# Kernel optimization log

Hardware: AMD Instinct MI355X
Metric: run time of the kernel (lower is better)

## Reference

```python
import jax, jax.numpy as jnp
import numpy as np

N = 10000
E = 320000
D_IN = 512
D_OUT = 256


def setup_inputs() -> dict:
    key = jax.random.key(0)
    ks = jax.random.split(key, 10)
    x = jax.random.normal(ks[0], (N, D_IN), dtype=jnp.float32)
    edge_index = jax.random.randint(ks[1], (2, E), 0, N, dtype=jnp.int64)
    s_in = 1.0 / np.sqrt(D_IN)
    s_out = 1.0 / np.sqrt(D_OUT)
    W0 = jax.random.uniform(ks[2], (D_IN, D_OUT), minval=-s_in, maxval=s_in, dtype=jnp.float32)
    b0 = jax.random.uniform(ks[3], (D_OUT,), minval=-s_in, maxval=s_in, dtype=jnp.float32)
    Wl1 = jax.random.uniform(ks[4], (D_OUT, D_OUT), minval=-s_out, maxval=s_out, dtype=jnp.float32)
    bl1 = jax.random.uniform(ks[5], (D_OUT,), minval=-s_out, maxval=s_out, dtype=jnp.float32)
    Wr1 = jax.random.uniform(ks[6], (D_OUT, D_OUT), minval=-s_out, maxval=s_out, dtype=jnp.float32)
    Wl2 = jax.random.uniform(ks[7], (D_OUT, D_OUT), minval=-s_out, maxval=s_out, dtype=jnp.float32)
    bl2 = jax.random.uniform(ks[8], (D_OUT,), minval=-s_out, maxval=s_out, dtype=jnp.float32)
    Wr2 = jax.random.uniform(ks[9], (D_OUT, D_OUT), minval=-s_out, maxval=s_out, dtype=jnp.float32)
    return {"x": x, "edge_index": edge_index, "W0": W0, "b0": b0,
            "Wl1": Wl1, "bl1": bl1, "Wr1": Wr1,
            "Wl2": Wl2, "bl2": bl2, "Wr2": Wr2}


def _sage_conv(h, src, dst, Wl, bl, Wr):
    # mean aggregation over incoming edges: msg j->i uses h[src], summed at dst
    msg = h[src]                                        # [E, D]
    agg = jax.ops.segment_sum(msg, dst, num_segments=N)  # [N, D]
    deg = jax.ops.segment_sum(jnp.ones((msg.shape[0],), h.dtype), dst, num_segments=N)
    mean = agg / jnp.maximum(deg, 1.0)[:, None]
    return mean @ Wl + bl + h @ Wr


def reference(x, edge_index, W0, b0, Wl1, bl1, Wr1, Wl2, bl2, Wr2):
    src, dst = edge_index[0], edge_index[1]
    h = x @ W0 + b0                 # lin; dropout = identity (eval mode)
    out1 = jax.nn.relu(_sage_conv(h, src, dst, Wl1, bl1, Wr1)) + h
    out2 = _sage_conv(out1, src, dst, Wl2, bl2, Wr2) + out1
    return (out1, out2)
```

## Files before the change

### kernel.cpp

```cpp
#include <hip/hip_runtime.h>
#include <cstdint>

#define N_NODES 10000
#define N_EDGES 320000
#define DIN 512
#define DOUT 256
#define DEG_CAP 96

using short8 = __attribute__((ext_vector_type(8))) short;
using f32x4  = __attribute__((ext_vector_type(4))) float;
typedef unsigned short ushort_t;

static __device__ __forceinline__ unsigned short f2bf(float f) {
  unsigned u = __builtin_bit_cast(unsigned, f);
  u += 0x7fffu + ((u >> 16) & 1u);
  return (unsigned short)(u >> 16);
}
static __device__ __forceinline__ float bf2f(unsigned short s) {
  unsigned u = ((unsigned)s) << 16;
  return __builtin_bit_cast(float, u);
}

static __device__ __forceinline__ int detect64(const unsigned* ei) {
  unsigned z = 0;
  #pragma unroll
  for (int i = 1; i < 32; i += 2) z |= ei[i];
  return z == 0u;
}
static __device__ __forceinline__ int load_idx(const unsigned* ei, int i, int is64) {
  return is64 ? (int)ei[2 * i] : (int)ei[i];
}

#define B_EDGE 1250
#define B_W    1536
#define B_X    5000
__global__ __launch_bounds__(256) void prep_all(
    const unsigned* __restrict__ ei, int* __restrict__ cnt,
    int* __restrict__ srcs,
    const float* __restrict__ x, ushort_t* __restrict__ xb,
    const float* __restrict__ W0,
    const float* __restrict__ Wl1, const float* __restrict__ Wr1,
    const float* __restrict__ Wl2, const float* __restrict__ Wr2,
    ushort_t* __restrict__ W0T, ushort_t* __restrict__ WT1,
    ushort_t* __restrict__ WT2) {
  int b = blockIdx.x;
  if (b < B_EDGE) {
    int is64 = detect64(ei);
    int e = b * 256 + threadIdx.x;
    int d = load_idx(ei, N_EDGES + e, is64);
    int s = load_idx(ei, e, is64);
    int pos = atomicAdd(&cnt[d], 1);
    if (pos < DEG_CAP) srcs[d * DEG_CAP + pos] = s;
  } else if (b < B_EDGE + B_W) {
    int g = (b - B_EDGE) * 256 + threadIdx.x;
    int mat = g >> 17;
    int r = g & 131071;
    int n = r >> 9, k = r & 511;
    float v;
    ushort_t* dst;
    if (mat == 0)      { v = W0[k * 256 + n]; dst = W0T; }
    else if (mat == 1) { v = (k < 256) ? Wl1[k * 256 + n] : Wr1[(k - 256) * 256 + n]; dst = WT1; }
    else               { v = (k < 256) ? Wl2[k * 256 + n] : Wr2[(k - 256) * 256 + n]; dst = WT2; }
    dst[r] = f2bf(v);
  } else {
    int g = (b - B_EDGE - B_W) * 256 + threadIdx.x;
    float4 f = *(const float4*)(x + (size_t)g * 4);
    uint2 o;
    o.x = (unsigned)f2bf(f.x) | ((unsigned)f2bf(f.y) << 16);
    o.y = (unsigned)f2bf(f.z) | ((unsigned)f2bf(f.w) << 16);
    *(uint2*)(xb + (size_t)g * 4) = o;
  }
}

__global__ __launch_bounds__(256) void agg_mean(const ushort_t* __restrict__ h,
                                                const int* __restrict__ cnt,
                                                const int* __restrict__ srcs,
                                                ushort_t* __restrict__ mean) {
  int node = blockIdx.x * 4 + (threadIdx.x >> 6);
  int lane = threadIdx.x & 63;
  if (node >= N_NODES) return;
  int deg = cnt[node];
  int d = (deg < DEG_CAP) ? deg : DEG_CAP;
  int beg = node * DEG_CAP;
  int end = beg + d;
  float a0 = 0.f, a1 = 0.f, a2 = 0.f, a3 = 0.f;
  int j = beg;
  for (; j + 16 <= end; j += 16) {
    int4 sa = *(const int4*)(srcs + j);
    int4 sb = *(const int4*)(srcs + j + 4);
    int4 sc = *(const int4*)(srcs + j + 8);
    int4 sd = *(const int4*)(srcs + j + 12);
    uint2 u0 = *(const uint2*)(h + (size_t)sa.x * 256 + lane * 4);
    uint2 u1 = *(const uint2*)(h + (size_t)sa.y * 256 + lane * 4);
    uint2 u2 = *(const uint2*)(h + (size_t)sa.z * 256 + lane * 4);
    uint2 u3 = *(const uint2*)(h + (size_t)sa.w * 256 + lane * 4);
    uint2 u4 = *(const uint2*)(h + (size_t)sb.x * 256 + lane * 4);
    uint2 u5 = *(const uint2*)(h + (size_t)sb.y * 256 + lane * 4);
    uint2 u6 = *(const uint2*)(h + (size_t)sb.z * 256 + lane * 4);
    uint2 u7 = *(const uint2*)(h + (size_t)sb.w * 256 + lane * 4);
    uint2 u8 = *(const uint2*)(h + (size_t)sc.x * 256 + lane * 4);
    uint2 u9 = *(const uint2*)(h + (size_t)sc.y * 256 + lane * 4);
    uint2 ua = *(const uint2*)(h + (size_t)sc.z * 256 + lane * 4);
    uint2 ub = *(const uint2*)(h + (size_t)sc.w * 256 + lane * 4);
    uint2 uc = *(const uint2*)(h + (size_t)sd.x * 256 + lane * 4);
    uint2 ud = *(const uint2*)(h + (size_t)sd.y * 256 + lane * 4);
    uint2 ue = *(const uint2*)(h + (size_t)sd.z * 256 + lane * 4);
    uint2 uf = *(const uint2*)(h + (size_t)sd.w * 256 + lane * 4);
    a0 += bf2f(u0.x & 0xffff) + bf2f(u1.x & 0xffff) + bf2f(u2.x & 0xffff) + bf2f(u3.x & 0xffff);
    a1 += bf2f(u0.x >> 16)    + bf2f(u1.x >> 16)    + bf2f(u2.x >> 16)    + bf2f(u3.x >> 16);
    a2 += bf2f(u0.y & 0xffff) + bf2f(u1.y & 0xffff) + bf2f(u2.y & 0xffff) + bf2f(u3.y & 0xffff);
    a3 += bf2f(u0.y >> 16)    + bf2f(u1.y >> 16)    + bf2f(u2.y >> 16)    + bf2f(u3.y >> 16);
    a0 += bf2f(u4.x & 0xffff) + bf2f(u5.x & 0xffff) + bf2f(u6.x & 0xffff) + bf2f(u7.x & 0xffff);
    a1 += bf2f(u4.x >> 16)    + bf2f(u5.x >> 16)    + bf2f(u6.x >> 16)    + bf2f(u7.x >> 16);
    a2 += bf2f(u4.y & 0xffff) + bf2f(u5.y & 0xffff) + bf2f(u6.y & 0xffff) + bf2f(u7.y & 0xffff);
    a3 += bf2f(u4.y >> 16)    + bf2f(u5.y >> 16)    + bf2f(u6.y >> 16)    + bf2f(u7.y >> 16);
    a0 += bf2f(u8.x & 0xffff) + bf2f(u9.x & 0xffff) + bf2f(ua.x & 0xffff) + bf2f(ub.x & 0xffff);
    a1 += bf2f(u8.x >> 16)    + bf2f(u9.x >> 16)    + bf2f(ua.x >> 16)    + bf2f(ub.x >> 16);
    a2 += bf2f(u8.y & 0xffff) + bf2f(u9.y & 0xffff) + bf2f(ua.y & 0xffff) + bf2f(ub.y & 0xffff);
    a3 += bf2f(u8.y >> 16)    + bf2f(u9.y >> 16)    + bf2f(ua.y >> 16)    + bf2f(ub.y >> 16);
    a0 += bf2f(uc.x & 0xffff) + bf2f(ud.x & 0xffff) + bf2f(ue.x & 0xffff) + bf2f(uf.x & 0xffff);
    a1 += bf2f(uc.x >> 16)    + bf2f(ud.x >> 16)    + bf2f(ue.x >> 16)    + bf2f(uf.x >> 16);
    a2 += bf2f(uc.y & 0xffff) + bf2f(ud.y & 0xffff) + bf2f(ue.y & 0xffff) + bf2f(uf.y & 0xffff);
    a3 += bf2f(uc.y >> 16)    + bf2f(ud.y >> 16)    + bf2f(ue.y >> 16)    + bf2f(uf.y >> 16);
  }
  for (; j + 8 <= end; j += 8) {
    int4 sa = *(const int4*)(srcs + j);
    int4 sb = *(const int4*)(srcs + j + 4);
    uint2 u0 = *(const uint2*)(h + (size_t)sa.x * 256 + lane * 4);
    uint2 u1 = *(const uint2*)(h + (size_t)sa.y * 256 + lane * 4);
    uint2 u2 = *(const uint2*)(h + (size_t)sa.z * 256 + lane * 4);
    uint2 u3 = *(const uint2*)(h + (size_t)sa.w * 256 + lane * 4);
    uint2 u4 = *(const uint2*)(h + (size_t)sb.x * 256 + lane * 4);
    uint2 u5 = *(const uint2*)(h + (size_t)sb.y * 256 + lane * 4);
    uint2 u6 = *(const uint2*)(h + (size_t)sb.z * 256 + lane * 4);
    uint2 u7 = *(const uint2*)(h + (size_t)sb.w * 256 + lane * 4);
    a0 += bf2f(u0.x & 0xffff) + bf2f(u1.x & 0xffff) + bf2f(u2.x & 0xffff) + bf2f(u3.x & 0xffff);
    a1 += bf2f(u0.x >> 16)    + bf2f(u1.x >> 16)    + bf2f(u2.x >> 16)    + bf2f(u3.x >> 16);
    a2 += bf2f(u0.y & 0xffff) + bf2f(u1.y & 0xffff) + bf2f(u2.y & 0xffff) + bf2f(u3.y & 0xffff);
    a3 += bf2f(u0.y >> 16)    + bf2f(u1.y >> 16)    + bf2f(u2.y >> 16)    + bf2f(u3.y >> 16);
    a0 += bf2f(u4.x & 0xffff) + bf2f(u5.x & 0xffff) + bf2f(u6.x & 0xffff) + bf2f(u7.x & 0xffff);
    a1 += bf2f(u4.x >> 16)    + bf2f(u5.x >> 16)    + bf2f(u6.x >> 16)    + bf2f(u7.x >> 16);
    a2 += bf2f(u4.y & 0xffff) + bf2f(u5.y & 0xffff) + bf2f(u6.y & 0xffff) + bf2f(u7.y & 0xffff);
    a3 += bf2f(u4.y >> 16)    + bf2f(u5.y >> 16)    + bf2f(u6.y >> 16)    + bf2f(u7.y >> 16);
  }
  for (; j + 4 <= end; j += 4) {
    int4 s4 = *(const int4*)(srcs + j);
    uint2 u0 = *(const uint2*)(h + (size_t)s4.x * 256 + lane * 4);
    uint2 u1 = *(const uint2*)(h + (size_t)s4.y * 256 + lane * 4);
    uint2 u2 = *(const uint2*)(h + (size_t)s4.z * 256 + lane * 4);
    uint2 u3 = *(const uint2*)(h + (size_t)s4.w * 256 + lane * 4);
    a0 += bf2f(u0.x & 0xffff) + bf2f(u1.x & 0xffff) + bf2f(u2.x & 0xffff) + bf2f(u3.x & 0xffff);
    a1 += bf2f(u0.x >> 16)    + bf2f(u1.x >> 16)    + bf2f(u2.x >> 16)    + bf2f(u3.x >> 16);
    a2 += bf2f(u0.y & 0xffff) + bf2f(u1.y & 0xffff) + bf2f(u2.y & 0xffff) + bf2f(u3.y & 0xffff);
    a3 += bf2f(u0.y >> 16)    + bf2f(u1.y >> 16)    + bf2f(u2.y >> 16)    + bf2f(u3.y >> 16);
  }
  for (; j < end; ++j) {
    int s0 = srcs[j];
    uint2 u0 = *(const uint2*)(h + (size_t)s0 * 256 + lane * 4);
    a0 += bf2f(u0.x & 0xffff);
    a1 += bf2f(u0.x >> 16);
    a2 += bf2f(u0.y & 0xffff);
    a3 += bf2f(u0.y >> 16);
  }
  float inv = 1.0f / (float)(d > 1 ? d : 1);
  a0 *= inv; a1 *= inv; a2 *= inv; a3 *= inv;
  uint2 o;
  o.x = (unsigned)f2bf(a0) | ((unsigned)f2bf(a1) << 16);
  o.y = (unsigned)f2bf(a2) | ((unsigned)f2bf(a3) << 16);
  *(uint2*)(mean + (size_t)node * 256 + lane * 4) = o;
}

template<int DO_RELU, int HAS_ADD, int HAS_OUTF, int HAS_OUTB, int SPLIT_A>
__global__ __launch_bounds__(256) void gemm_pan(
    const ushort_t* __restrict__ A0, const ushort_t* __restrict__ A1,
    const ushort_t* __restrict__ BT, const float* __restrict__ bias,
    const ushort_t* __restrict__ addB,
    float* __restrict__ outF, ushort_t* __restrict__ outB, int M) {
  __shared__ ushort_t Bs[64 * 520];

  const int bid = blockIdx.x;
  const int sg  = bid >> 5;
  const int r32 = bid & 31;
  const int xt  = (sg << 3) + (r32 & 7);
  const int yt  = r32 >> 3;
  const int xtiles = (M + 127) >> 7;
  if (xt >= xtiles) return;

  const int tid  = threadIdx.x;
  const int lane = tid & 63;
  const int w    = tid >> 6;
  const int bn   = yt * 64;
  const int mbase = xt * 128 + w * 32;

  #pragma unroll
  for (int i = 0; i < 16; ++i) {
    int c = i * 256 + tid;
    int row = c >> 6;
    int c8  = (c & 63) * 8;
    uint4 bv = *(const uint4*)(BT + (size_t)(bn + row) * 512 + c8);
    *(uint4*)&Bs[row * 520 + c8] = bv;
  }
  __syncthreads();

  f32x4 acc[2][4] = {};
  const int mrow = lane & 15;
  const int k8   = (lane >> 4) * 8;

  #pragma unroll
  for (int kt = 0; kt < 512; kt += 32) {
    const ushort_t* Asrc;
    int acol, ald;
    if (SPLIT_A) {
      if (kt < 256) { Asrc = A0; acol = kt; } else { Asrc = A1; acol = kt - 256; }
      ald = 256;
    } else {
      Asrc = A0; acol = kt; ald = 512;
    }
    short8 a[2], b[4];
    #pragma unroll
    for (int s = 0; s < 2; ++s) {
      int row = mbase + s * 16 + mrow;
      a[s] = *(const short8*)(Asrc + (size_t)row * ald + acol + k8);
    }
    #pragma unroll
    for (int ni = 0; ni < 4; ++ni)
      b[ni] = *(const short8*)&Bs[(ni * 16 + mrow) * 520 + kt + k8];
    #pragma unroll
    for (int s = 0; s < 2; ++s)
      #pragma unroll
      for (int ni = 0; ni < 4; ++ni)
        acc[s][ni] = __builtin_amdgcn_mfma_f32_16x16x32_bf16(a[s], b[ni], acc[s][ni], 0, 0, 0);
  }

  const int cq   = lane >> 4;
  const int ccol = lane & 15;
  #pragma unroll
  for (int ni = 0; ni < 4; ++ni) {
    int gcol = bn + ni * 16 + ccol;
    float bv = bias[gcol];
    #pragma unroll
    for (int s = 0; s < 2; ++s) {
      #pragma unroll
      for (int r = 0; r < 4; ++r) {
        int grow = mbase + s * 16 + cq * 4 + r;
        if (grow < M) {
          float v = acc[s][ni][r] + bv;
          if (DO_RELU) v = fmaxf(v, 0.f);
          if (HAS_ADD) v += bf2f(addB[(size_t)grow * DOUT + gcol]);
          if (HAS_OUTF) __builtin_nontemporal_store(v, &outF[(size_t)grow * DOUT + gcol]);
          if (HAS_OUTB) outB[(size_t)grow * DOUT + gcol] = f2bf(v);
        }
      }
    }
  }
}

extern "C" void kernel_launch(void* const* d_in, const int* in_sizes, int n_in,
                              void* d_out, int out_size, void* d_ws, size_t ws_size,
                              hipStream_t stream) {
  const float*    x   = (const float*)d_in[0];
  const unsigned* ei  = (const unsigned*)d_in[1];
  const float*    W0  = (const float*)d_in[2];
  const float*    b0  = (const float*)d_in[3];
  const float*    Wl1 = (const float*)d_in[4];
  const float*    bl1 = (const float*)d_in[5];
  const float*    Wr1 = (const float*)d_in[6];
  const float*    Wl2 = (const float*)d_in[7];
  const float*    bl2 = (const float*)d_in[8];
  const float*    Wr2 = (const float*)d_in[9];

  char* ws = (char*)d_ws;
  size_t off = 0;
  auto alloc = [&](size_t bytes) {
    char* p = ws + off;
    off += (bytes + 255) & ~(size_t)255;
    return p;
  };
  ushort_t* xb  = (ushort_t*)alloc((size_t)N_NODES * 512 * 2);
  ushort_t* hb  = (ushort_t*)alloc((size_t)N_NODES * 256 * 2);
  ushort_t* o1b = (ushort_t*)alloc((size_t)N_NODES * 256 * 2);
  ushort_t* mb  = (ushort_t*)alloc((size_t)N_NODES * 256 * 2);
  ushort_t* W0T = (ushort_t*)alloc(256 * 512 * 2);
  ushort_t* WT1 = (ushort_t*)alloc(256 * 512 * 2);
  ushort_t* WT2 = (ushort_t*)alloc(256 * 512 * 2);
  int* cnt    = (int*)alloc(N_NODES * 4);
  int* srcs   = (int*)alloc((size_t)N_NODES * DEG_CAP * 4);

  float* out1 = (float*)d_out;
  float* out2 = out1 + (size_t)N_NODES * DOUT;

  hipMemsetAsync(cnt, 0, N_NODES * 4, stream);
  prep_all<<<B_EDGE + B_W + B_X, 256, 0, stream>>>(ei, cnt, srcs, x, xb,
                                                   W0, Wl1, Wr1, Wl2, Wr2,
                                                   W0T, WT1, WT2);

  const int GG = 320;
  gemm_pan<0, 0, 0, 1, 0><<<GG, 256, 0, stream>>>(xb, nullptr, W0T, b0, nullptr,
                                                  nullptr, hb, N_NODES);
  agg_mean<<<(N_NODES + 3) / 4, 256, 0, stream>>>(hb, cnt, srcs, mb);
  gemm_pan<1, 1, 1, 1, 1><<<GG, 256, 0, stream>>>(mb, hb, WT1, bl1, hb,
                                                  out1, o1b, N_NODES);
  agg_mean<<<(N_NODES + 3) / 4, 256, 0, stream>>>(o1b, cnt, srcs, mb);
  gemm_pan<0, 1, 1, 0, 1><<<GG, 256, 0, stream>>>(mb, o1b, WT2, bl2, o1b,
                                                  out2, nullptr, N_NODES);
}
```

Baseline: 196.0 us.

## Fuse all stages into one persistent kernel with software grid barriers

Replaces the six separate launches (prep, three GEMMs, two aggregations) with a single persistent kernel of 512 blocks. The stages are separated by atomic-counter grid barriers, and the aggregation and prep loops become grid-stride loops. The GEMM now stages B in two K-halves of shared memory (264-stride) so two blocks can fit per CU. This removes per-launch overhead and tail gaps between kernels, at the cost of spin-wait barriers, the risk of deadlock if not all blocks are co-resident, and 192 of 512 blocks sitting idle during the GEMM phases.

```diff
diff --git a/kernel.cpp b/kernel.cpp
--- a/kernel.cpp
+++ b/kernel.cpp
@@ -6,6 +6,8 @@
 #define DIN 512
 #define DOUT 256
 #define DEG_CAP 96
+#define NBLK 512
+#define GTHREADS (NBLK * 256)
 
 using short8 = __attribute__((ext_vector_type(8))) short;
 using f32x4  = __attribute__((ext_vector_type(4))) float;
@@ -31,228 +33,231 @@
   return is64 ? (int)ei[2 * i] : (int)ei[i];
 }
 
-#define B_EDGE 1250
-#define B_W    1536
-#define B_X    5000
-__global__ __launch_bounds__(256) void prep_all(
-    const unsigned* __restrict__ ei, int* __restrict__ cnt,
-    int* __restrict__ srcs,
-    const float* __restrict__ x, ushort_t* __restrict__ xb,
-    const float* __restrict__ W0,
-    const float* __restrict__ Wl1, const float* __restrict__ Wr1,
-    const float* __restrict__ Wl2, const float* __restrict__ Wr2,
-    ushort_t* __restrict__ W0T, ushort_t* __restrict__ WT1,
-    ushort_t* __restrict__ WT2) {
-  int b = blockIdx.x;
-  if (b < B_EDGE) {
-    int is64 = detect64(ei);
-    int e = b * 256 + threadIdx.x;
-    int d = load_idx(ei, N_EDGES + e, is64);
-    int s = load_idx(ei, e, is64);
-    int pos = atomicAdd(&cnt[d], 1);
-    if (pos < DEG_CAP) srcs[d * DEG_CAP + pos] = s;
-  } else if (b < B_EDGE + B_W) {
-    int g = (b - B_EDGE) * 256 + threadIdx.x;
-    int mat = g >> 17;
-    int r = g & 131071;
-    int n = r >> 9, k = r & 511;
-    float v;
-    ushort_t* dst;
-    if (mat == 0)      { v = W0[k * 256 + n]; dst = W0T; }
-    else if (mat == 1) { v = (k < 256) ? Wl1[k * 256 + n] : Wr1[(k - 256) * 256 + n]; dst = WT1; }
-    else               { v = (k < 256) ? Wl2[k * 256 + n] : Wr2[(k - 256) * 256 + n]; dst = WT2; }
-    dst[r] = f2bf(v);
-  } else {
-    int g = (b - B_EDGE - B_W) * 256 + threadIdx.x;
-    float4 f = *(const float4*)(x + (size_t)g * 4);
-    uint2 o;
-    o.x = (unsigned)f2bf(f.x) | ((unsigned)f2bf(f.y) << 16);
-    o.y = (unsigned)f2bf(f.z) | ((unsigned)f2bf(f.w) << 16);
-    *(uint2*)(xb + (size_t)g * 4) = o;
+static __device__ __forceinline__ void grid_sync(int* bar, int ph) {
+  __syncthreads();
+  if (threadIdx.x == 0) {
+    __threadfence();
+    __hip_atomic_fetch_add(&bar[ph], 1, __ATOMIC_ACQ_REL, __HIP_MEMORY_SCOPE_AGENT);
+    while (__hip_atomic_load(&bar[ph], __ATOMIC_ACQUIRE, __HIP_MEMORY_SCOPE_AGENT) < NBLK)
+      __builtin_amdgcn_s_sleep(8);
+    __threadfence();
   }
-}
-
-__global__ __launch_bounds__(256) void agg_mean(const ushort_t* __restrict__ h,
-                                                const int* __restrict__ cnt,
-                                                const int* __restrict__ srcs,
-                                                ushort_t* __restrict__ mean) {
-  int node = blockIdx.x * 4 + (threadIdx.x >> 6);
-  int lane = threadIdx.x & 63;
-  if (node >= N_NODES) return;
-  int deg = cnt[node];
-  int d = (deg < DEG_CAP) ? deg : DEG_CAP;
-  int beg = node * DEG_CAP;
-  int end = beg + d;
-  float a0 = 0.f, a1 = 0.f, a2 = 0.f, a3 = 0.f;
-  int j = beg;
-  for (; j + 16 <= end; j += 16) {
-    int4 sa = *(const int4*)(srcs + j);
-    int4 sb = *(const int4*)(srcs + j + 4);
-    int4 sc = *(const int4*)(srcs + j + 8);
-    int4 sd = *(const int4*)(srcs + j + 12);
-    uint2 u0 = *(const uint2*)(h + (size_t)sa.x * 256 + lane * 4);
-    uint2 u1 = *(const uint2*)(h + (size_t)sa.y * 256 + lane * 4);
-    uint2 u2 = *(const uint2*)(h + (size_t)sa.z * 256 + lane * 4);
-    uint2 u3 = *(const uint2*)(h + (size_t)sa.w * 256 + lane * 4);
-    uint2 u4 = *(const uint2*)(h + (size_t)sb.x * 256 + lane * 4);
-    uint2 u5 = *(const uint2*)(h + (size_t)sb.y * 256 + lane * 4);
-    uint2 u6 = *(const uint2*)(h + (size_t)sb.z * 256 + lane * 4);
-    uint2 u7 = *(const uint2*)(h + (size_t)sb.w * 256 + lane * 4);
-    uint2 u8 = *(const uint2*)(h + (size_t)sc.x * 256 + lane * 4);
-    uint2 u9 = *(const uint2*)(h + (size_t)sc.y * 256 + lane * 4);
-    uint2 ua = *(const uint2*)(h + (size_t)sc.z * 256 + lane * 4);
-    uint2 ub = *(const uint2*)(h + (size_t)sc.w * 256 + lane * 4);
-    uint2 uc = *(const uint2*)(h + (size_t)sd.x * 256 + lane * 4);
-    uint2 ud = *(const uint2*)(h + (size_t)sd.y * 256 + lane * 4);
-    uint2 ue = *(const uint2*)(h + (size_t)sd.z * 256 + lane * 4);
-    uint2 uf = *(const uint2*)(h + (size_t)sd.w * 256 + lane * 4);
-    a0 += bf2f(u0.x & 0xffff) + bf2f(u1.x & 0xffff) + bf2f(u2.x & 0xffff) + bf2f(u3.x & 0xffff);
-    a1 += bf2f(u0.x >> 16)    + bf2f(u1.x >> 16)    + bf2f(u2.x >> 16)    + bf2f(u3.x >> 16);
-    a2 += bf2f(u0.y & 0xffff) + bf2f(u1.y & 0xffff) + bf2f(u2.y & 0xffff) + bf2f(u3.y & 0xffff);
-    a3 += bf2f(u0.y >> 16)    + bf2f(u1.y >> 16)    + bf2f(u2.y >> 16)    + bf2f(u3.y >> 16);
-    a0 += bf2f(u4.x & 0xffff) + bf2f(u5.x & 0xffff) + bf2f(u6.x & 0xffff) + bf2f(u7.x & 0xffff);
-    a1 += bf2f(u4.x >> 16)    + bf2f(u5.x >> 16)    + bf2f(u6.x >> 16)    + bf2f(u7.x >> 16);
-    a2 += bf2f(u4.y & 0xffff) + bf2f(u5.y & 0xffff) + bf2f(u6.y & 0xffff) + bf2f(u7.y & 0xffff);
-    a3 += bf2f(u4.y >> 16)    + bf2f(u5.y >> 16)    + bf2f(u6.y >> 16)    + bf2f(u7.y >> 16);
-    a0 += bf2f(u8.x & 0xffff) + bf2f(u9.x & 0xffff) + bf2f(ua.x & 0xffff) + bf2f(ub.x & 0xffff);
-    a1 += bf2f(u8.x >> 16)    + bf2f(u9.x >> 16)    + bf2f(ua.x >> 16)    + bf2f(ub.x >> 16);
-    a2 += bf2f(u8.y & 0xffff) + bf2f(u9.y & 0xffff) + bf2f(ua.y & 0xffff) + bf2f(ub.y & 0xffff);
-    a3 += bf2f(u8.y >> 16)    + bf2f(u9.y >> 16)    + bf2f(ua.y >> 16)    + bf2f(ub.y >> 16);
-    a0 += bf2f(uc.x & 0xffff) + bf2f(ud.x & 0xffff) + bf2f(ue.x & 0xffff) + bf2f(uf.x & 0xffff);
-    a1 += bf2f(uc.x >> 16)    + bf2f(ud.x >> 16)    + bf2f(ue.x >> 16)    + bf2f(uf.x >> 16);
-    a2 += bf2f(uc.y & 0xffff) + bf2f(ud.y & 0xffff) + bf2f(ue.y & 0xffff) + bf2f(uf.y & 0xffff);
-    a3 += bf2f(uc.y >> 16)    + bf2f(ud.y >> 16)    + bf2f(ue.y >> 16)    + bf2f(uf.y >> 16);
-  }
-  for (; j + 8 <= end; j += 8) {
-    int4 sa = *(const int4*)(srcs + j);
-    int4 sb = *(const int4*)(srcs + j + 4);
-    uint2 u0 = *(const uint2*)(h + (size_t)sa.x * 256 + lane * 4);
-    uint2 u1 = *(const uint2*)(h + (size_t)sa.y * 256 + lane * 4);
-    uint2 u2 = *(const uint2*)(h + (size_t)sa.z * 256 + lane * 4);
-    uint2 u3 = *(const uint2*)(h + (size_t)sa.w * 256 + lane * 4);
-    uint2 u4 = *(const uint2*)(h + (size_t)sb.x * 256 + lane * 4);
-    uint2 u5 = *(const uint2*)(h + (size_t)sb.y * 256 + lane * 4);
-    uint2 u6 = *(const uint2*)(h + (size_t)sb.z * 256 + lane * 4);
-    uint2 u7 = *(const uint2*)(h + (size_t)sb.w * 256 + lane * 4);
-    a0 += bf2f(u0.x & 0xffff) + bf2f(u1.x & 0xffff) + bf2f(u2.x & 0xffff) + bf2f(u3.x & 0xffff);
-    a1 += bf2f(u0.x >> 16)    + bf2f(u1.x >> 16)    + bf2f(u2.x >> 16)    + bf2f(u3.x >> 16);
-    a2 += bf2f(u0.y & 0xffff) + bf2f(u1.y & 0xffff) + bf2f(u2.y & 0xffff) + bf2f(u3.y & 0xffff);
-    a3 += bf2f(u0.y >> 16)    + bf2f(u1.y >> 16)    + bf2f(u2.y >> 16)    + bf2f(u3.y >> 16);
-    a0 += bf2f(u4.x & 0xffff) + bf2f(u5.x & 0xffff) + bf2f(u6.x & 0xffff) + bf2f(u7.x & 0xffff);
-    a1 += bf2f(u4.x >> 16)    + bf2f(u5.x >> 16)    + bf2f(u6.x >> 16)    + bf2f(u7.x >> 16);
-    a2 += bf2f(u4.y & 0xffff) + bf2f(u5.y & 0xffff) + bf2f(u6.y & 0xffff) + bf2f(u7.y & 0xffff);
-    a3 += bf2f(u4.y >> 16)    + bf2f(u5.y >> 16)    + bf2f(u6.y >> 16)    + bf2f(u7.y >> 16);
-  }
-  for (; j + 4 <= end; j += 4) {
-    int4 s4 = *(const int4*)(srcs + j);
-    uint2 u0 = *(const uint2*)(h + (size_t)s4.x * 256 + lane * 4);
-    uint2 u1 = *(const uint2*)(h + (size_t)s4.y * 256 + lane * 4);
-    uint2 u2 = *(const uint2*)(h + (size_t)s4.z * 256 + lane * 4);
-    uint2 u3 = *(const uint2*)(h + (size_t)s4.w * 256 + lane * 4);
-    a0 += bf2f(u0.x & 0xffff) + bf2f(u1.x & 0xffff) + bf2f(u2.x & 0xffff) + bf2f(u3.x & 0xffff);
-    a1 += bf2f(u0.x >> 16)    + bf2f(u1.x >> 16)    + bf2f(u2.x >> 16)    + bf2f(u3.x >> 16);
-    a2 += bf2f(u0.y & 0xffff) + bf2f(u1.y & 0xffff) + bf2f(u2.y & 0xffff) + bf2f(u3.y & 0xffff);
-    a3 += bf2f(u0.y >> 16)    + bf2f(u1.y >> 16)    + bf2f(u2.y >> 16)    + bf2f(u3.y >> 16);
-  }
-  for (; j < end; ++j) {
-    int s0 = srcs[j];
-    uint2 u0 = *(const uint2*)(h + (size_t)s0 * 256 + lane * 4);
-    a0 += bf2f(u0.x & 0xffff);
-    a1 += bf2f(u0.x >> 16);
-    a2 += bf2f(u0.y & 0xffff);
-    a3 += bf2f(u0.y >> 16);
-  }
-  float inv = 1.0f / (float)(d > 1 ? d : 1);
-  a0 *= inv; a1 *= inv; a2 *= inv; a3 *= inv;
-  uint2 o;
-  o.x = (unsigned)f2bf(a0) | ((unsigned)f2bf(a1) << 16);
-  o.y = (unsigned)f2bf(a2) | ((unsigned)f2bf(a3) << 16);
-  *(uint2*)(mean + (size_t)node * 256 + lane * 4) = o;
-}
-
-template<int DO_RELU, int HAS_ADD, int HAS_OUTF, int HAS_OUTB, int SPLIT_A>
-__global__ __launch_bounds__(256) void gemm_pan(
+  __syncthreads();
+}
+
+template<int RELU, int ADD, int OUTF, int OUTB, int SPLIT>
+static __device__ __forceinline__ void gemm_phase(
     const ushort_t* __restrict__ A0, const ushort_t* __restrict__ A1,
     const ushort_t* __restrict__ BT, const float* __restrict__ bias,
     const ushort_t* __restrict__ addB,
-    float* __restrict__ outF, ushort_t* __restrict__ outB, int M) {
-  __shared__ ushort_t Bs[64 * 520];
-
+    float* __restrict__ outF, ushort_t* __restrict__ outB, ushort_t* Bs) {
   const int bid = blockIdx.x;
-  const int sg  = bid >> 5;
-  const int r32 = bid & 31;
-  const int xt  = (sg << 3) + (r32 & 7);
-  const int yt  = r32 >> 3;
-  const int xtiles = (M + 127) >> 7;
-  if (xt >= xtiles) return;
-
-  const int tid  = threadIdx.x;
-  const int lane = tid & 63;
-  const int w    = tid >> 6;
-  const int bn   = yt * 64;
-  const int mbase = xt * 128 + w * 32;
-
-  #pragma unroll
-  for (int i = 0; i < 16; ++i) {
-    int c = i * 256 + tid;
-    int row = c >> 6;
-    int c8  = (c & 63) * 8;
-    uint4 bv = *(const uint4*)(BT + (size_t)(bn + row) * 512 + c8);
-    *(uint4*)&Bs[row * 520 + c8] = bv;
-  }
-  __syncthreads();
-
-  f32x4 acc[2][4] = {};
-  const int mrow = lane & 15;
-  const int k8   = (lane >> 4) * 8;
-
-  #pragma unroll
-  for (int kt = 0; kt < 512; kt += 32) {
-    const ushort_t* Asrc;
-    int acol, ald;
-    if (SPLIT_A) {
-      if (kt < 256) { Asrc = A0; acol = kt; } else { Asrc = A1; acol = kt - 256; }
-      ald = 256;
-    } else {
-      Asrc = A0; acol = kt; ald = 512;
-    }
-    short8 a[2], b[4];
+  if (bid < 320) {
+    const int sg  = bid >> 5;
+    const int r32 = bid & 31;
+    const int xt  = (sg << 3) + (r32 & 7);
+    const int yt  = r32 >> 3;
+    const int tid  = threadIdx.x;
+    const int lane = tid & 63;
+    const int w    = tid >> 6;
+    const int bn   = yt * 64;
+    const int mbase = xt * 128 + w * 32;
+
+    f32x4 acc[2][4] = {};
+    const int mrow = lane & 15;
+    const int k8   = (lane >> 4) * 8;
+    const int cq   = lane >> 4;
+    const int ccol = lane & 15;
+
     #pragma unroll
-    for (int s = 0; s < 2; ++s) {
-      int row = mbase + s * 16 + mrow;
-      a[s] = *(const short8*)(Asrc + (size_t)row * ald + acol + k8);
-    }
+    for (int hh = 0; hh < 2; ++hh) {
+      if (hh) __syncthreads();
+      #pragma unroll
+      for (int i = 0; i < 8; ++i) {
+        int c = i * 256 + tid;
+        int row = c >> 5;
+        int c8  = (c & 31) * 8;
+        uint4 bv = *(const uint4*)(BT + (size_t)(bn + row) * 512 + hh * 256 + c8);
+        *(uint4*)&Bs[row * 264 + c8] = bv;
+      }
+      __syncthreads();
+
+      const ushort_t* Asrc = SPLIT ? (hh ? A1 : A0) : A0;
+      const int ald  = SPLIT ? 256 : 512;
+      const int abase = SPLIT ? 0 : hh * 256;
+      #pragma unroll
+      for (int kt = 0; kt < 256; kt += 32) {
+        short8 a[2], b[4];
+        #pragma unroll
+        for (int s = 0; s < 2; ++s) {
+          int row = mbase + s * 16 + mrow;
+          a[s] = *(const short8*)(Asrc + (size_t)row * ald + abase + kt + k8);
+        }
+        #pragma unroll
+        for (int ni = 0; ni < 4; ++ni)
+          b[ni] = *(const short8*)&Bs[(ni * 16 + mrow) * 264 + kt + k8];
+        #pragma unroll
+        for (int s = 0; s < 2; ++s)
+          #pragma unroll
+          for (int ni = 0; ni < 4; ++ni)
+            acc[s][ni] = __builtin_amdgcn_mfma_f32_16x16x32_bf16(a[s], b[ni], acc[s][ni], 0, 0, 0);
+      }
+    }
+
     #pragma unroll
-    for (int ni = 0; ni < 4; ++ni)
-      b[ni] = *(const short8*)&Bs[(ni * 16 + mrow) * 520 + kt + k8];
-    #pragma unroll
-    for (int s = 0; s < 2; ++s)
+    for (int ni = 0; ni < 4; ++ni) {
+      int gcol = bn + ni * 16 + ccol;
+      float bv = bias[gcol];
       #pragma unroll
-      for (int ni = 0; ni < 4; ++ni)
-        acc[s][ni] = __builtin_amdgcn_mfma_f32_16x16x32_bf16(a[s], b[ni], acc[s][ni], 0, 0, 0);
-  }
-
-  const int cq   = lane >> 4;
-  const int ccol = lane & 15;
-  #pragma unroll
-  for (int ni = 0; ni < 4; ++ni) {
-    int gcol = bn + ni * 16 + ccol;
-    float bv = bias[gcol];
-    #pragma unroll
-    for (int s = 0; s < 2; ++s) {
-      #pragma unroll
-      for (int r = 0; r < 4; ++r) {
-        int grow = mbase + s * 16 + cq * 4 + r;
-        if (grow < M) {
-          float v = acc[s][ni][r] + bv;
-          if (DO_RELU) v = fmaxf(v, 0.f);
-          if (HAS_ADD) v += bf2f(addB[(size_t)grow * DOUT + gcol]);
-          if (HAS_OUTF) __builtin_nontemporal_store(v, &outF[(size_t)grow * DOUT + gcol]);
-          if (HAS_OUTB) outB[(size_t)grow * DOUT + gcol] = f2bf(v);
+      for (int s = 0; s < 2; ++s) {
+        #pragma unroll
+        for (int r = 0; r < 4; ++r) {
+          int grow = mbase + s * 16 + cq * 4 + r;
+          if (grow < N_NODES) {
+            size_t idx = (size_t)grow * DOUT + gcol;
+            float v = acc[s][ni][r] + bv;
+            if (RELU) v = fmaxf(v, 0.f);
+            if (ADD)  v += bf2f(addB[idx]);
+            if (OUTF) __builtin_nontemporal_store(v, &outF[idx]);
+            if (OUTB) outB[idx] = f2bf(v);
+          }
         }
       }
     }
   }
+}
+
+static __device__ __forceinline__ void agg_phase(
+    const ushort_t* __restrict__ h, const int* __restrict__ cnt,
+    const int* __restrict__ srcs, ushort_t* __restrict__ mean) {
+  const int lane = threadIdx.x & 63;
+  for (int grp = blockIdx.x; grp < 2500; grp += NBLK) {
+    int node = grp * 4 + (threadIdx.x >> 6);
+    int deg = cnt[node];
+    int d = (deg < DEG_CAP) ? deg : DEG_CAP;
+    int beg = node * DEG_CAP;
+    int end = beg + d;
+    float a0 = 0.f, a1 = 0.f, a2 = 0.f, a3 = 0.f;
+    int j = beg;
+    for (; j + 16 <= end; j += 16) {
+      int4 sa = *(const int4*)(srcs + j);
+      int4 sb = *(const int4*)(srcs + j + 4);
+      int4 sc = *(const int4*)(srcs + j + 8);
+      int4 sd = *(const int4*)(srcs + j + 12);
+      uint2 u0 = *(const uint2*)(h + (size_t)sa.x * 256 + lane * 4);
+      uint2 u1 = *(const uint2*)(h + (size_t)sa.y * 256 + lane * 4);
+      uint2 u2 = *(const uint2*)(h + (size_t)sa.z * 256 + lane * 4);
+      uint2 u3 = *(const uint2*)(h + (size_t)sa.w * 256 + lane * 4);
+      uint2 u4 = *(const uint2*)(h + (size_t)sb.x * 256 + lane * 4);
+      uint2 u5 = *(const uint2*)(h + (size_t)sb.y * 256 + lane * 4);
+      uint2 u6 = *(const uint2*)(h + (size_t)sb.z * 256 + lane * 4);
+      uint2 u7 = *(const uint2*)(h + (size_t)sb.w * 256 + lane * 4);
+      uint2 u8 = *(const uint2*)(h + (size_t)sc.x * 256 + lane * 4);
+      uint2 u9 = *(const uint2*)(h + (size_t)sc.y * 256 + lane * 4);
+      uint2 ua = *(const uint2*)(h + (size_t)sc.z * 256 + lane * 4);
+      uint2 ub = *(const uint2*)(h + (size_t)sc.w * 256 + lane * 4);
+      uint2 uc = *(const uint2*)(h + (size_t)sd.x * 256 + lane * 4);
+      uint2 ud = *(const uint2*)(h + (size_t)sd.y * 256 + lane * 4);
+      uint2 ue = *(const uint2*)(h + (size_t)sd.z * 256 + lane * 4);
+      uint2 uf = *(const uint2*)(h + (size_t)sd.w * 256 + lane * 4);
+      a0 += bf2f(u0.x & 0xffff) + bf2f(u1.x & 0xffff) + bf2f(u2.x & 0xffff) + bf2f(u3.x & 0xffff);
+      a1 += bf2f(u0.x >> 16)    + bf2f(u1.x >> 16)    + bf2f(u2.x >> 16)    + bf2f(u3.x >> 16);
+      a2 += bf2f(u0.y & 0xffff) + bf2f(u1.y & 0xffff) + bf2f(u2.y & 0xffff) + bf2f(u3.y & 0xffff);
+      a3 += bf2f(u0.y >> 16)    + bf2f(u1.y >> 16)    + bf2f(u2.y >> 16)    + bf2f(u3.y >> 16);
+      a0 += bf2f(u4.x & 0xffff) + bf2f(u5.x & 0xffff) + bf2f(u6.x & 0xffff) + bf2f(u7.x & 0xffff);
+      a1 += bf2f(u4.x >> 16)    + bf2f(u5.x >> 16)    + bf2f(u6.x >> 16)    + bf2f(u7.x >> 16);
+      a2 += bf2f(u4.y & 0xffff) + bf2f(u5.y & 0xffff) + bf2f(u6.y & 0xffff) + bf2f(u7.y & 0xffff);
+      a3 += bf2f(u4.y >> 16)    + bf2f(u5.y >> 16)    + bf2f(u6.y >> 16)    + bf2f(u7.y >> 16);
+      a0 += bf2f(u8.x & 0xffff) + bf2f(u9.x & 0xffff) + bf2f(ua.x & 0xffff) + bf2f(ub.x & 0xffff);
+      a1 += bf2f(u8.x >> 16)    + bf2f(u9.x >> 16)    + bf2f(ua.x >> 16)    + bf2f(ub.x >> 16);
+      a2 += bf2f(u8.y & 0xffff) + bf2f(u9.y & 0xffff) + bf2f(ua.y & 0xffff) + bf2f(ub.y & 0xffff);
+      a3 += bf2f(u8.y >> 16)    + bf2f(u9.y >> 16)    + bf2f(ua.y >> 16)    + bf2f(ub.y >> 16);
+      a0 += bf2f(uc.x & 0xffff) + bf2f(ud.x & 0xffff) + bf2f(ue.x & 0xffff) + bf2f(uf.x & 0xffff);
+      a1 += bf2f(uc.x >> 16)    + bf2f(ud.x >> 16)    + bf2f(ue.x >> 16)    + bf2f(uf.x >> 16);
+      a2 += bf2f(uc.y & 0xffff) + bf2f(ud.y & 0xffff) + bf2f(ue.y & 0xffff) + bf2f(uf.y & 0xffff);
+      a3 += bf2f(uc.y >> 16)    + bf2f(ud.y >> 16)    + bf2f(ue.y >> 16)    + bf2f(uf.y >> 16);
+    }
+    for (; j + 4 <= end; j += 4) {
+      int4 s4 = *(const int4*)(srcs + j);
+      uint2 u0 = *(const uint2*)(h + (size_t)s4.x * 256 + lane * 4);
+      uint2 u1 = *(const uint2*)(h + (size_t)s4.y * 256 + lane * 4);
+      uint2 u2 = *(const uint2*)(h + (size_t)s4.z * 256 + lane * 4);
+      uint2 u3 = *(const uint2*)(h + (size_t)s4.w * 256 + lane * 4);
+      a0 += bf2f(u0.x & 0xffff) + bf2f(u1.x & 0xffff) + bf2f(u2.x & 0xffff) + bf2f(u3.x & 0xffff);
+      a1 += bf2f(u0.x >> 16)    + bf2f(u1.x >> 16)    + bf2f(u2.x >> 16)    + bf2f(u3.x >> 16);
+      a2 += bf2f(u0.y & 0xffff) + bf2f(u1.y & 0xffff) + bf2f(u2.y & 0xffff) + bf2f(u3.y & 0xffff);
+      a3 += bf2f(u0.y >> 16)    + bf2f(u1.y >> 16)    + bf2f(u2.y >> 16)    + bf2f(u3.y >> 16);
+    }
+    for (; j < end; ++j) {
+      int s0 = srcs[j];
+      uint2 u0 = *(const uint2*)(h + (size_t)s0 * 256 + lane * 4);
+      a0 += bf2f(u0.x & 0xffff);
+      a1 += bf2f(u0.x >> 16);
+      a2 += bf2f(u0.y & 0xffff);
+      a3 += bf2f(u0.y >> 16);
+    }
+    float inv = 1.0f / (float)(d > 1 ? d : 1);
+    a0 *= inv; a1 *= inv; a2 *= inv; a3 *= inv;
+    uint2 o;
+    o.x = (unsigned)f2bf(a0) | ((unsigned)f2bf(a1) << 16);
+    o.y = (unsigned)f2bf(a2) | ((unsigned)f2bf(a3) << 16);
+    *(uint2*)(mean + (size_t)node * 256 + lane * 4) = o;
+  }
+}
+
+__global__ __launch_bounds__(256, 2) void mega(
+    const float* __restrict__ x, const unsigned* __restrict__ ei,
+    const float* __restrict__ W0, const float* __restrict__ b0,
+    const float* __restrict__ Wl1, const float* __restrict__ bl1,
+    const float* __restrict__ Wr1,
+    const float* __restrict__ Wl2, const float* __restrict__ bl2,
+    const float* __restrict__ Wr2,
+    ushort_t* __restrict__ xb, ushort_t* __restrict__ hb,
+    ushort_t* __restrict__ o1b, ushort_t* __restrict__ mb,
+    ushort_t* __restrict__ W0T, ushort_t* __restrict__ WT1,
+    ushort_t* __restrict__ WT2,
+    int* __restrict__ cnt, int* __restrict__ srcs, int* __restrict__ bar,
+    float* __restrict__ out1, float* __restrict__ out2) {
+  __shared__ ushort_t Bs[64 * 264];
+  const int gtid = blockIdx.x * 256 + threadIdx.x;
+
+  {
+    int is64 = detect64(ei);
+    for (int e = gtid; e < N_EDGES; e += GTHREADS) {
+      int d = load_idx(ei, N_EDGES + e, is64);
+      int s = load_idx(ei, e, is64);
+      int pos = atomicAdd(&cnt[d], 1);
+      if (pos < DEG_CAP) srcs[d * DEG_CAP + pos] = s;
+    }
+    for (int g = gtid; g < 3 * 131072; g += GTHREADS) {
+      int mat = g >> 17;
+      int r = g & 131071;
+      int n = r >> 9, k = r & 511;
+      float v;
+      ushort_t* dst;
+      if (mat == 0)      { v = W0[k * 256 + n]; dst = W0T; }
+      else if (mat == 1) { v = (k < 256) ? Wl1[k * 256 + n] : Wr1[(k - 256) * 256 + n]; dst = WT1; }
+      else               { v = (k < 256) ? Wl2[k * 256 + n] : Wr2[(k - 256) * 256 + n]; dst = WT2; }
+      dst[r] = f2bf(v);
+    }
+    for (int g = gtid; g < 1280000; g += GTHREADS) {
+      float4 f = *(const float4*)(x + (size_t)g * 4);
+      uint2 o;
+      o.x = (unsigned)f2bf(f.x) | ((unsigned)f2bf(f.y) << 16);
+      o.y = (unsigned)f2bf(f.z) | ((unsigned)f2bf(f.w) << 16);
+      *(uint2*)(xb + (size_t)g * 4) = o;
+    }
+  }
+  grid_sync(bar, 0);
+  gemm_phase<0, 0, 0, 1, 0>(xb, nullptr, W0T, b0, nullptr, nullptr, hb, Bs);
+  grid_sync(bar, 1);
+  agg_phase(hb, cnt, srcs, mb);
+  grid_sync(bar, 2);
+  gemm_phase<1, 1, 1, 1, 1>(mb, hb, WT1, bl1, hb, out1, o1b, Bs);
+  grid_sync(bar, 3);
+  agg_phase(o1b, cnt, srcs, mb);
+  grid_sync(bar, 4);
+  gemm_phase<0, 1, 1, 0, 1>(mb, o1b, WT2, bl2, o1b, out2, nullptr, Bs);
 }
 
 extern "C" void kernel_launch(void* const* d_in, const int* in_sizes, int n_in,
@@ -283,24 +288,16 @@
   ushort_t* W0T = (ushort_t*)alloc(256 * 512 * 2);
   ushort_t* WT1 = (ushort_t*)alloc(256 * 512 * 2);
   ushort_t* WT2 = (ushort_t*)alloc(256 * 512 * 2);
-  int* cnt    = (int*)alloc(N_NODES * 4);
-  int* srcs   = (int*)alloc((size_t)N_NODES * DEG_CAP * 4);
+  int* cnt  = (int*)alloc(N_NODES * 4);
+  int* bar  = (int*)alloc(64);
+  int* srcs = (int*)alloc((size_t)N_EDGES ? (size_t)N_NODES * DEG_CAP * 4 : 0);
 
   float* out1 = (float*)d_out;
   float* out2 = out1 + (size_t)N_NODES * DOUT;
 
-  hipMemsetAsync(cnt, 0, N_NODES * 4, stream);
-  prep_all<<<B_EDGE + B_W + B_X, 256, 0, stream>>>(ei, cnt, srcs, x, xb,
-                                                   W0, Wl1, Wr1, Wl2, Wr2,
-                                                   W0T, WT1, WT2);
-
-  const int GG = 320;
-  gemm_pan<0, 0, 0, 1, 0><<<GG, 256, 0, stream>>>(xb, nullptr, W0T, b0, nullptr,
-                                                  nullptr, hb, N_NODES);
-  agg_mean<<<(N_NODES + 3) / 4, 256, 0, stream>>>(hb, cnt, srcs, mb);
-  gemm_pan<1, 1, 1, 1, 1><<<GG, 256, 0, stream>>>(mb, hb, WT1, bl1, hb,
-                                                  out1, o1b, N_NODES);
-  agg_mean<<<(N_NODES + 3) / 4, 256, 0, stream>>>(o1b, cnt, srcs, mb);
-  gemm_pan<0, 1, 1, 0, 1><<<GG, 256, 0, stream>>>(mb, o1b, WT2, bl2, o1b,
-                                                  out2, nullptr, N_NODES);
-}
+  hipMemsetAsync(cnt, 0, (size_t)((char*)bar - (char*)cnt) + 64, stream);
+
+  mega<<<NBLK, 256, 0, stream>>>(x, ei, W0, b0, Wl1, bl1, Wr1, Wl2, bl2, Wr2,
+                                 xb, hb, o1b, mb, W0T, WT1, WT2,
+                                 cnt, srcs, bar, out1, out2);
+}
```

New measurement: 725.8 us. 270% more time.

## Fuse x fp32-to-bf16 conversion into first GEMM and halve GEMM N-tile

Applied to the files above, without the earlier changes.

The separate x-to-bf16 conversion blocks are removed from the prep kernel, and the first GEMM now reads fp32 x directly and converts it to bf16 in registers, which saves a full write and re-read of a 10 MB intermediate. The GEMM tile shrinks from 64 to 32 output columns, with a smaller shared B panel, twice as many blocks and a launch bound of 4 blocks per SM, to raise occupancy and parallelism. The 8-edge unroll stage in the aggregation kernel is dropped. The trade-off is that each block re-reads the A rows from global memory twice as often, and the fp32 A loads double the bytes fetched per element in the first GEMM.

```diff
diff --git a/kernel.cpp b/kernel.cpp
--- a/kernel.cpp
+++ b/kernel.cpp
@@ -33,11 +33,9 @@
 
 #define B_EDGE 1250
 #define B_W    1536
-#define B_X    5000
 __global__ __launch_bounds__(256) void prep_all(
     const unsigned* __restrict__ ei, int* __restrict__ cnt,
     int* __restrict__ srcs,
-    const float* __restrict__ x, ushort_t* __restrict__ xb,
     const float* __restrict__ W0,
     const float* __restrict__ Wl1, const float* __restrict__ Wr1,
     const float* __restrict__ Wl2, const float* __restrict__ Wr2,
@@ -51,7 +49,7 @@
     int s = load_idx(ei, e, is64);
     int pos = atomicAdd(&cnt[d], 1);
     if (pos < DEG_CAP) srcs[d * DEG_CAP + pos] = s;
-  } else if (b < B_EDGE + B_W) {
+  } else {
     int g = (b - B_EDGE) * 256 + threadIdx.x;
     int mat = g >> 17;
     int r = g & 131071;
@@ -62,13 +60,6 @@
     else if (mat == 1) { v = (k < 256) ? Wl1[k * 256 + n] : Wr1[(k - 256) * 256 + n]; dst = WT1; }
     else               { v = (k < 256) ? Wl2[k * 256 + n] : Wr2[(k - 256) * 256 + n]; dst = WT2; }
     dst[r] = f2bf(v);
-  } else {
-    int g = (b - B_EDGE - B_W) * 256 + threadIdx.x;
-    float4 f = *(const float4*)(x + (size_t)g * 4);
-    uint2 o;
-    o.x = (unsigned)f2bf(f.x) | ((unsigned)f2bf(f.y) << 16);
-    o.y = (unsigned)f2bf(f.z) | ((unsigned)f2bf(f.w) << 16);
-    *(uint2*)(xb + (size_t)g * 4) = o;
   }
 }
 
@@ -123,26 +114,6 @@
     a2 += bf2f(uc.y & 0xffff) + bf2f(ud.y & 0xffff) + bf2f(ue.y & 0xffff) + bf2f(uf.y & 0xffff);
     a3 += bf2f(uc.y >> 16)    + bf2f(ud.y >> 16)    + bf2f(ue.y >> 16)    + bf2f(uf.y >> 16);
   }
-  for (; j + 8 <= end; j += 8) {
-    int4 sa = *(const int4*)(srcs + j);
-    int4 sb = *(const int4*)(srcs + j + 4);
-    uint2 u0 = *(const uint2*)(h + (size_t)sa.x * 256 + lane * 4);
-    uint2 u1 = *(const uint2*)(h + (size_t)sa.y * 256 + lane * 4);
-    uint2 u2 = *(const uint2*)(h + (size_t)sa.z * 256 + lane * 4);
-    uint2 u3 = *(const uint2*)(h + (size_t)sa.w * 256 + lane * 4);
-    uint2 u4 = *(const uint2*)(h + (size_t)sb.x * 256 + lane * 4);
-    uint2 u5 = *(const uint2*)(h + (size_t)sb.y * 256 + lane * 4);
-    uint2 u6 = *(const uint2*)(h + (size_t)sb.z * 256 + lane * 4);
-    uint2 u7 = *(const uint2*)(h + (size_t)sb.w * 256 + lane * 4);
-    a0 += bf2f(u0.x & 0xffff) + bf2f(u1.x & 0xffff) + bf2f(u2.x & 0xffff) + bf2f(u3.x & 0xffff);
-    a1 += bf2f(u0.x >> 16)    + bf2f(u1.x >> 16)    + bf2f(u2.x >> 16)    + bf2f(u3.x >> 16);
-    a2 += bf2f(u0.y & 0xffff) + bf2f(u1.y & 0xffff) + bf2f(u2.y & 0xffff) + bf2f(u3.y & 0xffff);
-    a3 += bf2f(u0.y >> 16)    + bf2f(u1.y >> 16)    + bf2f(u2.y >> 16)    + bf2f(u3.y >> 16);
-    a0 += bf2f(u4.x & 0xffff) + bf2f(u5.x & 0xffff) + bf2f(u6.x & 0xffff) + bf2f(u7.x & 0xffff);
-    a1 += bf2f(u4.x >> 16)    + bf2f(u5.x >> 16)    + bf2f(u6.x >> 16)    + bf2f(u7.x >> 16);
-    a2 += bf2f(u4.y & 0xffff) + bf2f(u5.y & 0xffff) + bf2f(u6.y & 0xffff) + bf2f(u7.y & 0xffff);
-    a3 += bf2f(u4.y >> 16)    + bf2f(u5.y >> 16)    + bf2f(u6.y >> 16)    + bf2f(u7.y >> 16);
-  }
   for (; j + 4 <= end; j += 4) {
     int4 s4 = *(const int4*)(srcs + j);
     uint2 u0 = *(const uint2*)(h + (size_t)s4.x * 256 + lane * 4);
@@ -170,30 +141,30 @@
   *(uint2*)(mean + (size_t)node * 256 + lane * 4) = o;
 }
 
-template<int DO_RELU, int HAS_ADD, int HAS_OUTF, int HAS_OUTB, int SPLIT_A>
-__global__ __launch_bounds__(256) void gemm_pan(
-    const ushort_t* __restrict__ A0, const ushort_t* __restrict__ A1,
+template<int AF32, int DO_RELU, int HAS_ADD, int HAS_OUTF, int HAS_OUTB, int SPLIT_A>
+__global__ __launch_bounds__(256, 4) void gemm_pan(
+    const void* __restrict__ Av0, const ushort_t* __restrict__ A1,
     const ushort_t* __restrict__ BT, const float* __restrict__ bias,
     const ushort_t* __restrict__ addB,
     float* __restrict__ outF, ushort_t* __restrict__ outB, int M) {
-  __shared__ ushort_t Bs[64 * 520];
+  __shared__ ushort_t Bs[32 * 520];
 
   const int bid = blockIdx.x;
-  const int sg  = bid >> 5;
-  const int r32 = bid & 31;
-  const int xt  = (sg << 3) + (r32 & 7);
-  const int yt  = r32 >> 3;
+  const int sg  = bid >> 6;
+  const int r64 = bid & 63;
+  const int xt  = (sg << 3) + (r64 & 7);
+  const int yt  = r64 >> 3;
   const int xtiles = (M + 127) >> 7;
   if (xt >= xtiles) return;
 
   const int tid  = threadIdx.x;
   const int lane = tid & 63;
   const int w    = tid >> 6;
-  const int bn   = yt * 64;
+  const int bn   = yt * 32;
   const int mbase = xt * 128 + w * 32;
 
   #pragma unroll
-  for (int i = 0; i < 16; ++i) {
+  for (int i = 0; i < 8; ++i) {
     int c = i * 256 + tid;
     int row = c >> 6;
     int c8  = (c & 63) * 8;
@@ -202,40 +173,61 @@
   }
   __syncthreads();
 
-  f32x4 acc[2][4] = {};
+  f32x4 acc[2][2] = {};
   const int mrow = lane & 15;
   const int k8   = (lane >> 4) * 8;
 
+  int arow[2];
+  #pragma unroll
+  for (int s = 0; s < 2; ++s) {
+    int rr = mbase + s * 16 + mrow;
+    arow[s] = AF32 ? (rr < M ? rr : M - 1) : rr;
+  }
+
   #pragma unroll
   for (int kt = 0; kt < 512; kt += 32) {
-    const ushort_t* Asrc;
-    int acol, ald;
-    if (SPLIT_A) {
-      if (kt < 256) { Asrc = A0; acol = kt; } else { Asrc = A1; acol = kt - 256; }
-      ald = 256;
-    } else {
-      Asrc = A0; acol = kt; ald = 512;
+    const ushort_t* Asrc = nullptr;
+    int acol = 0, ald = 0;
+    if (!AF32) {
+      if (SPLIT_A) {
+        if (kt < 256) { Asrc = (const ushort_t*)Av0; acol = kt; }
+        else          { Asrc = A1; acol = kt - 256; }
+        ald = 256;
+      } else {
+        Asrc = (const ushort_t*)Av0; acol = kt; ald = 512;
+      }
     }
-    short8 a[2], b[4];
+    short8 a[2], b[2];
     #pragma unroll
     for (int s = 0; s < 2; ++s) {
-      int row = mbase + s * 16 + mrow;
-      a[s] = *(const short8*)(Asrc + (size_t)row * ald + acol + k8);
+      if (AF32) {
+        const float* p = (const float*)Av0 + (size_t)arow[s] * 512 + kt + k8;
+        float4 f0 = *(const float4*)p;
+        float4 f1 = *(const float4*)(p + 4);
+        short8 av;
+        av[0] = (short)f2bf(f0.x); av[1] = (short)f2bf(f0.y);
+        av[2] = (short)f2bf(f0.z); av[3] = (short)f2bf(f0.w);
+        av[4] = (short)f2bf(f1.x); av[5] = (short)f2bf(f1.y);
+        av[6] = (short)f2bf(f1.z); av[7] = (short)f2bf(f1.w);
+        a[s] = av;
+      } else {
+        a[s] = *(const short8*)(Asrc + (size_t)arow[s] * ald + acol + k8);
+      }
     }
     #pragma unroll
-    for (int ni = 0; ni < 4; ++ni)
+    for (int ni = 0; ni < 2; ++ni)
       b[ni] = *(const short8*)&Bs[(ni * 16 + mrow) * 520 + kt + k8];
     #pragma unroll
     for (int s = 0; s < 2; ++s)
       #pragma unroll
-      for (int ni = 0; ni < 4; ++ni)
+      for (int ni = 0; ni < 2; ++ni)
         acc[s][ni] = __builtin_amdgcn_mfma_f32_16x16x32_bf16(a[s], b[ni], acc[s][ni], 0, 0, 0);
   }
 
   const int cq   = lane >> 4;
   const int ccol = lane & 15;
   #pragma unroll
-  for (int ni = 0; ni < 4; ++ni) {
+  for (int ni = 0; ni < 2; ++ni) {
     int gcol = bn + ni * 16 + ccol;
     float bv = bias[gcol];
     #pragma unroll
@@ -276,7 +268,6 @@
     off += (bytes + 255) & ~(size_t)255;
     return p;
   };
-  ushort_t* xb  = (ushort_t*)alloc((size_t)N_NODES * 512 * 2);
   ushort_t* hb  = (ushort_t*)alloc((size_t)N_NODES * 256 * 2);
   ushort_t* o1b = (ushort_t*)alloc((size_t)N_NODES * 256 * 2);
   ushort_t* mb  = (ushort_t*)alloc((size_t)N_NODES * 256 * 2);
@@ -290,17 +281,17 @@
   float* out2 = out1 + (size_t)N_NODES * DOUT;
 
   hipMemsetAsync(cnt, 0, N_NODES * 4, stream);
-  prep_all<<<B_EDGE + B_W + B_X, 256, 0, stream>>>(ei, cnt, srcs, x, xb,
-                                                   W0, Wl1, Wr1, Wl2, Wr2,
-                                                   W0T, WT1, WT2);
-
-  const int GG = 320;
-  gemm_pan<0, 0, 0, 1, 0><<<GG, 256, 0, stream>>>(xb, nullptr, W0T, b0, nullptr,
-                                                  nullptr, hb, N_NODES);
+  prep_all<<<B_EDGE + B_W, 256, 0, stream>>>(ei, cnt, srcs,
+                                             W0, Wl1, Wr1, Wl2, Wr2,
+                                             W0T, WT1, WT2);
+
+  const int GG = 640;
+  gemm_pan<1, 0, 0, 0, 1, 0><<<GG, 256, 0, stream>>>(x, nullptr, W0T, b0,
+                                                     nullptr, nullptr, hb, N_NODES);
   agg_mean<<<(N_NODES + 3) / 4, 256, 0, stream>>>(hb, cnt, srcs, mb);
-  gemm_pan<1, 1, 1, 1, 1><<<GG, 256, 0, stream>>>(mb, hb, WT1, bl1, hb,
-                                                  out1, o1b, N_NODES);
+  gemm_pan<0, 1, 1, 1, 1, 1><<<GG, 256, 0, stream>>>(mb, hb, WT1, bl1, hb,
+                                                     out1, o1b, N_NODES);
   agg_mean<<<(N_NODES + 3) / 4, 256, 0, stream>>>(o1b, cnt, srcs, mb);
-  gemm_pan<0, 1, 1, 0, 1><<<GG, 256, 0, stream>>>(mb, o1b, WT2, bl2, o1b,
-                                                  out2, nullptr, N_NODES);
-}
+  gemm_pan<0, 0, 1, 1, 0, 1><<<GG, 256, 0, stream>>>(mb, o1b, WT2, bl2, o1b,
+                                                     out2, nullptr, N_NODES);
+}
```

New measurement: 203.8 us. 1.04x slower.
